# Optimization experiments

Hardware: AMD Instinct MI355X
Metric: run time of the kernel (lower is better)

The kernel has to match this reference:

```python
import jax, jax.numpy as jnp
import numpy as np
from jax import lax

E = 10        # embed_dim
SEQ = 4000    # input_frame (sample_length=40)
G = 800       # group
F = 5         # frames_in_group
B = 16
VOCAB = 8192


def _conv2d(x, w, b):
    # x: [B, C, H, W], w: [O, I, 3, 3], padding=1 -> SAME
    y = lax.conv_general_dilated(x, w, (1, 1), 'SAME',
                                 dimension_numbers=('NCHW', 'OIHW', 'NCHW'))
    return y + b[None, :, None, None]


def _conv1d_k1(x, w, b):
    # Conv1d(seq, seq, kernel=1): x [B, S, L], w [S_out, S_in]
    return jnp.einsum('oi,bil->bol', w, x) + b[None, :, None]


def _linear(x, w, b):
    # torch Linear: w [out, in]
    return x @ w.T + b


def setup_inputs() -> dict:
    key = jax.random.key(0)
    ks = jax.random.split(key, 24)
    s = 0.02
    inp = {
        'X': jax.random.randint(ks[0], (B, SEQ, 15), 0, VOCAB),
        'emb_table': jax.random.normal(ks[1], (VOCAB, E), jnp.float32),
        'w_dwc_lsp': jax.random.normal(ks[2], (G, G, 3, 3), jnp.float32) * s,
        'b_dwc_lsp': jnp.zeros((G,), jnp.float32),
        'w_dwc_other': jax.random.normal(ks[3], (G, G, 3, 3), jnp.float32) * s,
        'b_dwc_other': jnp.zeros((G,), jnp.float32),
        'w_local': jax.random.normal(ks[4], (SEQ, SEQ), jnp.float32) * s,
        'b_local': jnp.zeros((SEQ,), jnp.float32),
        'w_global': jax.random.normal(ks[5], (SEQ, SEQ), jnp.float32) * s,
        'b_global': jnp.zeros((SEQ,), jnp.float32),
        'w_gq': jax.random.normal(ks[6], (4 * E, 4 * E), jnp.float32) * s,
        'b_gq': jnp.zeros((4 * E,), jnp.float32),
        'w_cq': jax.random.normal(ks[7], (4 * E, 4 * E), jnp.float32) * s,
        'b_cq': jnp.zeros((4 * E,), jnp.float32),
        'w_pq': jax.random.normal(ks[8], (4 * E, 3 * E), jnp.float32) * s,
        'b_pq': jnp.zeros((4 * E,), jnp.float32),
        'w_lk': jax.random.normal(ks[9], (4 * E, 4 * E), jnp.float32) * s,
        'b_lk': jnp.zeros((4 * E,), jnp.float32),
        'w_lv': jax.random.normal(ks[10], (4 * E, 4 * E), jnp.float32) * s,
        'b_lv': jnp.zeros((4 * E,), jnp.float32),
        'w_cls': jax.random.normal(ks[11], (1, SEQ * 4 * E * 3), jnp.float32) * 0.001,
        'b_cls': jnp.zeros((1,), jnp.float32),
        'bn_w': jnp.ones((1,), jnp.float32),
        'bn_b': jnp.zeros((1,), jnp.float32),
    }
    return inp


def reference(X, emb_table, w_dwc_lsp, b_dwc_lsp, w_dwc_other, b_dwc_other,
              w_local, b_local, w_global, b_global,
              w_gq, b_gq, w_cq, b_cq, w_pq, b_pq,
              w_lk, b_lk, w_lv, b_lv, w_cls, b_cls, bn_w, bn_b):
    batch, seq, cw = X.shape
    gamma = jnp.float32(0.8)
    pk = jnp.array([0, 0, 0, 0, 1, 3, 1, 2, 3, 2, 3, 1, 2, 3, 3], jnp.float32)
    D = jnp.repeat(gamma ** pk, E)  # [150]

    Xe = emb_table[X].reshape(batch, seq, cw * E) * D  # [B, S, 150]
    ch = Xe.reshape(batch, seq, cw, E)                  # 15 chunks of E

    lsp = ch[:, :, jnp.array([0, 1, 2, 3])].reshape(batch, seq, 4 * E)
    pitch = ch[:, :, jnp.array([4, 5, 10])].reshape(batch, seq, 3 * E)
    code = ch[:, :, jnp.array([6, 7, 11, 12])].reshape(batch, seq, 4 * E)
    gain = ch[:, :, jnp.array([8, 13, 9, 14])].reshape(batch, seq, 4 * E)

    conv_lsp = _conv2d(lsp.reshape(batch, G, F, 4 * E), w_dwc_lsp, b_dwc_lsp).reshape(batch, seq, 4 * E)
    conv_pitch = _conv2d(pitch.reshape(batch, G, F, 3 * E), w_dwc_other, b_dwc_other).reshape(batch, seq, 3 * E)
    conv_code = _conv2d(code.reshape(batch, G, F, 4 * E), w_dwc_other, b_dwc_other).reshape(batch, seq, 4 * E)
    conv_gain = _conv2d(gain.reshape(batch, G, F, 4 * E), w_dwc_other, b_dwc_other).reshape(batch, seq, 4 * E)

    conv_lsp = _conv1d_k1(conv_lsp, w_local, b_local)
    conv_pitch = _conv1d_k1(conv_pitch, w_local, b_local)
    conv_code = _conv1d_k1(conv_code, w_local, b_local)
    conv_gain = _conv1d_k1(conv_gain, w_local, b_local)

    gain_q = _linear(conv_gain, w_gq, b_gq)    # [B, S, 40]
    pitch_q = _linear(conv_pitch, w_pq, b_pq)  # [B, S, 40]
    code_q = _linear(conv_code, w_cq, b_cq)    # [B, S, 40]
    lsp_k = _linear(conv_lsp, w_lk, b_lk)
    lsp_v = _linear(conv_lsp, w_lv, b_lv)

    # Q @ K^T @ V with no softmax: associate as Q @ (K^T V), O(S*d^2)
    kv = jnp.einsum('bsd,bse->bde', lsp_k, lsp_v)  # [B, 40, 40]
    out_gain = jnp.einsum('bsd,bde->bse', gain_q, kv) + lsp
    out_pitch = jnp.einsum('bsd,bde->bse', pitch_q, kv) + lsp
    out_code = jnp.einsum('bsd,bde->bse', code_q, kv) + lsp

    atten_out = jnp.concatenate([out_gain, out_pitch, out_code], -1)  # [B, S, 120]
    gf = _conv1d_k1(atten_out, w_global, b_global).reshape(batch, -1)  # [B, 480000]

    y = gf @ w_cls.T + b_cls  # [B, 1]
    # BatchNorm1d(1) in eval mode: running_mean=0, running_var=1
    eps = jnp.float32(1e-5)
    y = y * (bn_w / jnp.sqrt(1.0 + eps)) + bn_b
    return jax.nn.sigmoid(y)
```

## Files before the change

kernel.cpp:

```cpp
#include <hip/hip_runtime.h>
#include <hip/hip_bf16.h>

typedef _Float16 f16;
typedef __attribute__((ext_vector_type(8))) _Float16 half8;
typedef __attribute__((ext_vector_type(4))) _Float16 half4;
typedef __attribute__((ext_vector_type(4))) float f32x4;

static const int BN = 16, SEQN = 4000;

__device__ __forceinline__ void gload_lds(f16* lds, const f16* g) {
  __builtin_amdgcn_global_load_lds((const __attribute__((address_space(1))) unsigned int*)g,
                                   (__attribute__((address_space(3))) unsigned int*)lds, 16, 0, 0);
}

__device__ __forceinline__ int xcd_swz(int orig, int nwg) {
  int q = nwg >> 3, r = nwg & 7, x = orig & 7, o = orig >> 3;
  return (x < r ? x * (q + 1) : r * (q + 1) + (x - r) * q) + o;
}

__device__ __forceinline__ void body_wconv(char* SM, int o,
    const float* __restrict__ w_dwc_l, f16* __restrict__ wp_lsp) {
  float* sh = (float*)SM;
  int t = threadIdx.x;
  for (int p4 = t; p4 < 1800; p4 += 256)
    *(f32x4*)&sh[p4 * 4] = *(const f32x4*)&w_dwc_l[(long)o * 7200 + p4 * 4];
  __syncthreads();
  for (int p = t; p < 7296; p += 256) {
    int seg = p / 2432, r = p - seg * 2432;
    f16 v = (f16)0.f;
    if (r < 2400) { int de = r / 800, gi = r - de * 800; v = (f16)sh[gi * 9 + seg * 3 + de]; }
    wp_lsp[(long)o * 7296 + p] = v;
  }
}

__device__ __forceinline__ void body_wlocal(char* SM, int s,
    const float* __restrict__ w_local, f16* __restrict__ wlp) {
  float* sh = (float*)SM;
  int t = threadIdx.x;
  for (int p = t; p < 4000; p += 256) {
    int g = p / 5, f = p - g * 5;
    sh[f * 808 + g] = w_local[(long)s * 4000 + p];
  }
  __syncthreads();
  for (int p = t; p < 4096; p += 256) {
    f16 v = (f16)0.f;
    if (p < 4000) { int f = p / 800, g = p - f * 800; v = (f16)sh[f * 808 + g]; }
    wlp[(long)s * 4096 + p] = v;
  }
}

__device__ __forceinline__ void body_wcT(char* SM, int id,
    const float* __restrict__ w_cls, f16* __restrict__ wcT) {
  float (*tile)[33] = (float(*)[33])SM;
  int t = threadIdx.x;
  int c0 = (id % 4) * 32, r0 = (id / 4) * 32;
  int tx = t & 31, ty = t >> 5;
  for (int i = ty; i < 32; i += 8) {
    int r = r0 + i, c = c0 + tx;
    tile[i][tx] = (r < 4000 && c < 120) ? w_cls[(long)r * 120 + c] : 0.f;
  }
  __syncthreads();
  for (int i = ty; i < 32; i += 8) {
    int c = c0 + i, r = r0 + tx;
    if (c < 128 && r < 4000) wcT[(long)c * 4000 + r] = (f16)(tile[tx][i] * 1024.f);
  }
}

__device__ __forceinline__ void body_woT(char* SM, int id,
    const float* __restrict__ in, f16* __restrict__ out) {
  float (*sh)[293] = (float(*)[293])SM;
  int bg = id % 25, bgi = id / 25;
  int g0 = bg * 32, gi0 = bgi * 32;
  int t = threadIdx.x;
  for (int p = t; p < 2304; p += 256) {
    int gl = p / 72, q4 = p % 72;
    *(f32x4*)&sh[gl][q4 * 4] = *(const f32x4*)&in[(long)(g0 + gl) * 7200 + gi0 * 9 + q4 * 4];
  }
  __syncthreads();
  for (int p = t; p < 9216; p += 256) {
    int gl = p & 31, q = p >> 5;
    int gil = q & 31, z = q >> 5;
    out[(long)z * 640000 + (gi0 + gil) * 800 + g0 + gl] = (f16)sh[gl][gil * 9 + z];
  }
}

__device__ __forceinline__ void body_gather(char* SM, int bid,
    const int* __restrict__ X, const float* __restrict__ emb,
    f16* __restrict__ P_lsp, f16* __restrict__ P_pit,
    f16* __restrict__ P_cod, f16* __restrict__ P_gai,
    float* __restrict__ lsp32) {
  int* sx_ = (int*)SM;
  float* slsp = (float*)(SM + 9600);
  const float scale[15] = {1.f,1.f,1.f,1.f,0.8f,0.512f,0.8f,0.64f,0.512f,0.64f,0.512f,0.8f,0.64f,0.512f,0.512f};
  const int br[15] = {0,0,0,0,1,1,2,2,3,3,1,2,2,3,3};
  const int po[15] = {0,1,2,3,0,1,0,1,0,2,2,2,3,1,3};
  int t = threadIdx.x;
  int b = bid / 25, gc = bid % 25;
  int g0 = gc * 32, s0 = g0 * 5;
  const int* xbase = X + ((long)b * SEQN + s0) * 15;
  for (int p = t; p < 600; p += 256)
    *(f32x4*)&sx_[p * 4] = *(const f32x4*)&xbase[p * 4];
  __syncthreads();
  for (int it = t; it < 2400; it += 256) {
    int gl = it & 31, q = it >> 5, f = q % 5, c = q / 5;
    int idx = sx_[(gl * 5 + f) * 15 + c];
    const float* er = emb + (long)idx * 10;
    int ty = br[c], p = po[c];
    f16* P = (ty == 0) ? P_lsp : (ty == 1) ? P_pit : (ty == 2) ? P_cod : P_gai;
    int Wp = (ty == 1) ? 32 : 42;
    f16* base = P + ((long)((f + 1) * 16 + b) * Wp + (1 + p * 10)) * 800 + g0 + gl;
    float sc = scale[c];
#pragma unroll
    for (int j = 0; j < 10; j++) {
      float v = er[j] * sc;
      base[(long)j * 800] = (f16)v;
      if (ty == 0) slsp[(gl * 5 + f) * 41 + p * 10 + j] = v;
    }
  }
  __syncthreads();
  float* ldst = lsp32 + ((long)b * SEQN + s0) * 40;
  for (int p = t; p < 6400; p += 256) {
    int row = p / 40, col = p - row * 40;
    ldst[p] = slsp[row * 41 + col];
  }
}

__device__ __forceinline__ void body_c1(char* SM, int blk,
    const float* __restrict__ wcls, const float* __restrict__ bg,
    float* __restrict__ c1p) {
  float* red = (float*)SM;
  int t = threadIdx.x;
  float s = 0.f;
  for (long i = (long)blk * 256 + t; i < 480000; i += (long)120 * 256)
    s += wcls[i] * bg[i / 120];
  red[t] = s; __syncthreads();
  for (int o = 128; o > 0; o >>= 1) { if (t < o) red[t] += red[t + o]; __syncthreads(); }
  if (t == 0) c1p[blk] = red[0];
}

__device__ __forceinline__ void body_conv(char* SM, int id,
    const f16* __restrict__ P, const f16* __restrict__ wp, f16* __restrict__ Cp) {
  f16* Asb = (f16*)SM;
  f16* Bsb = Asb + 8192;
  int lin = xcd_swz(id % 175, 175);
  int z = id / 175;
  int df = z >> 1, hf = z & 1;
  int nx = lin % 7, my = lin / 7;
  int m0 = my * 128, n0 = nx * 128;
  Cp += (long)z * 2560000;
  int t = threadIdx.x;
  int gslot = (t & 3) ^ ((t >> 3) & 3);
  const f16 *ap[2], *bp[2];
#pragma unroll
  for (int q = 0; q < 2; q++) {
    int row = q * 64 + (t >> 2);
    int m = m0 + row;
    int f = m / 640, rem = m % 640, b = rem / 40, e = rem % 40;
    ap[q] = P + ((long)((f + df) * 16 + b) * 42 + e) * 800 + hf * 1216 + gslot * 8;
    bp[q] = wp + (long)(n0 + row) * 7296 + df * 2432 + hf * 1216 + gslot * 8;
  }
  int lane = t & 63, wv = t >> 6, l15 = lane & 15, kg = lane >> 4;
  int wm = (wv >> 1) * 64, wn = (wv & 1) * 64;
  int so = (kg ^ ((l15 >> 1) & 3)) << 3;
  f32x4 acc[4][4] = {};
  gload_lds(&Asb[t * 8], ap[0]); gload_lds(&Asb[2048 + t * 8], ap[1]);
  gload_lds(&Bsb[t * 8], bp[0]); gload_lds(&Bsb[2048 + t * 8], bp[1]);
  __syncthreads();
  int cur = 0;
  for (int kt = 0; kt < 38; kt++) {
    if (kt + 1 < 38) {
      int o = (kt + 1) * 32, nb = cur ^ 1;
      gload_lds(&Asb[nb * 4096 + t * 8], ap[0] + o); gload_lds(&Asb[nb * 4096 + 2048 + t * 8], ap[1] + o);
      gload_lds(&Bsb[nb * 4096 + t * 8], bp[0] + o); gload_lds(&Bsb[nb * 4096 + 2048 + t * 8], bp[1] + o);
    }
    half8 av[4], bv[4];
#pragma unroll
    for (int i = 0; i < 4; i++) av[i] = *(const half8*)&Asb[cur * 4096 + (wm + i * 16 + l15) * 32 + so];
#pragma unroll
    for (int j = 0; j < 4; j++) bv[j] = *(const half8*)&Bsb[cur * 4096 + (wn + j * 16 + l15) * 32 + so];
#pragma unroll
    for (int i = 0; i < 4; i++)
#pragma unroll
      for (int j = 0; j < 4; j++)
        acc[i][j] = __builtin_amdgcn_mfma_f32_16x16x32_f16(av[i], bv[j], acc[i][j], 0, 0, 0);
    __syncthreads();
    cur ^= 1;
  }
#pragma unroll
  for (int i = 0; i < 4; i++) {
    int mb = m0 + wm + i * 16 + kg * 4;
#pragma unroll
    for (int j = 0; j < 4; j++) {
      int n = n0 + wn + j * 16 + l15;
      if (n >= 800) continue;
      f32x4 d = acc[i][j];
#pragma unroll
      for (int r = 0; r < 4; r++)
        Cp[(long)(mb + r) * 800 + n] = (f16)d[r];
    }
  }
}

template <int OUTF16>
__device__ __forceinline__ void body_gemm128(char* SM, int x, int ky, int z,
    const f16* __restrict__ A, int lda, const f16* __restrict__ Bm, int ldb,
    float* __restrict__ C, f16* __restrict__ C16, int ldc,
    int gx, int nwg, int nkt, int KTtot, long cslice, long az, long bz, long cz,
    int Mreal, int Nreal, int Aclamp) {
  f16* Asb = (f16*)SM;
  f16* Bsb = Asb + 8192;
  A += (long)z * az;
  Bm += (long)z * bz;
  if (OUTF16) C16 += (long)z * cz + (long)ky * cslice;
  else C += (long)z * cz + (long)ky * cslice;
  int lin = xcd_swz(x, nwg);
  int nx = lin % gx, my = lin / gx;
  int m0 = my * 128, n0 = nx * 128;
  int kt0 = ky * nkt;
  int ktn = nkt; if (kt0 + ktn > KTtot) ktn = KTtot - kt0;
  int t = threadIdx.x;
  int gslot = (t & 3) ^ ((t >> 3) & 3);
  const f16 *ap[2], *bp[2];
#pragma unroll
  for (int q = 0; q < 2; q++) {
    int row = q * 64 + (t >> 2);
    int ra = m0 + row; if (ra >= Aclamp) ra = Aclamp - 1;
    ap[q] = A + (long)ra * lda + (long)kt0 * 32 + gslot * 8;
    bp[q] = Bm + (long)(n0 + row) * ldb + (long)kt0 * 32 + gslot * 8;
  }
  int lane = t & 63, wv = t >> 6, l15 = lane & 15, kg = lane >> 4;
  int wm = (wv >> 1) * 64, wn = (wv & 1) * 64;
  int so = (kg ^ ((l15 >> 1) & 3)) << 3;
  f32x4 acc[4][4] = {};
  gload_lds(&Asb[t * 8], ap[0]); gload_lds(&Asb[2048 + t * 8], ap[1]);
  gload_lds(&Bsb[t * 8], bp[0]); gload_lds(&Bsb[2048 + t * 8], bp[1]);
  __syncthreads();
  int cur = 0;
  for (int kt = 0; kt < ktn; kt++) {
    if (kt + 1 < ktn) {
      int o = (kt + 1) * 32, nb = cur ^ 1;
      gload_lds(&Asb[nb * 4096 + t * 8], ap[0] + o); gload_lds(&Asb[nb * 4096 + 2048 + t * 8], ap[1] + o);
      gload_lds(&Bsb[nb * 4096 + t * 8], bp[0] + o); gload_lds(&Bsb[nb * 4096 + 2048 + t * 8], bp[1] + o);
    }
    half8 av[4], bv[4];
#pragma unroll
    for (int i = 0; i < 4; i++) av[i] = *(const half8*)&Asb[cur * 4096 + (wm + i * 16 + l15) * 32 + so];
#pragma unroll
    for (int j = 0; j < 4; j++) bv[j] = *(const half8*)&Bsb[cur * 4096 + (wn + j * 16 + l15) * 32 + so];
#pragma unroll
    for (int i = 0; i < 4; i++)
#pragma unroll
      for (int j = 0; j < 4; j++)
        acc[i][j] = __builtin_amdgcn_mfma_f32_16x16x32_f16(av[i], bv[j], acc[i][j], 0, 0, 0);
    __syncthreads();
    cur ^= 1;
  }
#pragma unroll
  for (int i = 0; i < 4; i++) {
    int mb = m0 + wm + i * 16 + kg * 4;
#pragma unroll
    for (int j = 0; j < 4; j++) {
      int n = n0 + wn + j * 16 + l15;
      if (n >= Nreal) continue;
      f32x4 d = acc[i][j];
#pragma unroll
      for (int r = 0; r < 4; r++) {
        int m = mb + r;
        if (m >= Mreal) continue;
        if (OUTF16) C16[(long)m * ldc + n] = (f16)d[r];
        else C[(long)m * ldc + n] = d[r];
      }
    }
  }
}

__device__ __forceinline__ void body_tn(char* SM, int id,
    const f16* __restrict__ A, int lda, const float* __restrict__ B,
    const f16* __restrict__ B16, int ldb,
    float* __restrict__ C, int ldc, int nkt, int KTtot, long cslice,
    int Mreal, int Nreal) {
  f16* As = (f16*)SM;
  f16* Bs = As + 4096;
  int n0 = (id & 31) * 128;
  int ky = id >> 5;
  int kt0 = ky * nkt;
  int ktn = nkt; if (kt0 + ktn > KTtot) ktn = KTtot - kt0;
  C += (long)ky * cslice;
  int t = threadIdx.x;
  int gslot = (t & 3) ^ ((t >> 3) & 3);
  const f16 *ap0, *ap1;
  {
    int r0 = t >> 2, r1 = 64 + (t >> 2);
    if (r0 >= Mreal) r0 = Mreal - 1;
    if (r1 >= Mreal) r1 = Mreal - 1;
    ap0 = A + (long)r0 * lda + (long)kt0 * 32 + gslot * 8;
    ap1 = A + (long)r1 * lda + (long)kt0 * 32 + gslot * 8;
  }
  int lane = t & 63, wv = t >> 6;
  int wm = (wv >> 1) * 64, wn = (wv & 1) * 64;
  int l15 = lane & 15, kg = lane >> 4;
  int so = (kg ^ ((l15 >> 1) & 3)) << 3;
  f32x4 acc[4][4] = {};
  for (int kt = 0; kt < ktn; kt++) {
    f16 rb[4][4];
    int nli[4], kqi[4];
#pragma unroll
    for (int i = 0; i < 4; i++) {
      int idd = i * 256 + t;
      nli[i] = idd & 127; kqi[i] = idd >> 7;
      int gn = n0 + nli[i]; if (gn >= Nreal) gn = Nreal - 1;
      long kb = ((long)(kt0 + kt) * 32 + kqi[i] * 4);
#pragma unroll
      for (int j = 0; j < 4; j++)
        rb[i][j] = B16 ? B16[(kb + j) * ldb + gn] : (f16)B[(kb + j) * ldb + gn];
    }
    __syncthreads();
    gload_lds(&As[t * 8], ap0 + kt * 32);
    gload_lds(&As[2048 + t * 8], ap1 + kt * 32);
#pragma unroll
    for (int i = 0; i < 4; i++) {
      half4 h = {rb[i][0], rb[i][1], rb[i][2], rb[i][3]};
      *(half4*)&Bs[nli[i] * 36 + kqi[i] * 4] = h;
    }
    __syncthreads();
    half8 av[4], bv[4];
#pragma unroll
    for (int i = 0; i < 4; i++) {
      av[i] = *(const half8*)(&As[(wm + i * 16 + l15) * 32 + so]);
      bv[i] = *(const half8*)(&Bs[(wn + i * 16 + l15) * 36 + kg * 8]);
    }
#pragma unroll
    for (int i = 0; i < 4; i++)
#pragma unroll
      for (int j = 0; j < 4; j++)
        acc[i][j] = __builtin_amdgcn_mfma_f32_16x16x32_f16(av[i], bv[j], acc[i][j], 0, 0, 0);
  }
#pragma unroll
  for (int i = 0; i < 4; i++) {
    int mb = wm + i * 16 + kg * 4;
#pragma unroll
    for (int j = 0; j < 4; j++) {
      int n = n0 + wn + j * 16 + l15;
      if (n >= Nreal) continue;
      f32x4 d = acc[i][j];
#pragma unroll
      for (int r = 0; r < 4; r++) {
        int m = mb + r;
        if (m >= Mreal) continue;
        C[(long)m * ldc + n] = d[r];
      }
    }
  }
}

__device__ __forceinline__ void body_co_red(long gid,
    const f16* __restrict__ Cp, const float* __restrict__ bias, f16* __restrict__ co) {
  if (gid >= 640000) return;
  int m = gid / 200, n4 = (gid % 200) * 4;
  long o = (long)m * 800 + n4;
  f32x4 s = *(const f32x4*)&bias[n4];
#pragma unroll
  for (int z = 0; z < 6; z++) {
    half4 h = *(const half4*)&Cp[(long)z * 2560000 + o];
    s += (f32x4){(float)h[0], (float)h[1], (float)h[2], (float)h[3]};
  }
  int f = m / 640, r2 = m % 640;
  half4 hh = {(f16)s[0], (f16)s[1], (f16)s[2], (f16)s[3]};
  *(half4*)&co[(long)r2 * 4000 + f * 800 + n4] = hh;
}

__device__ __forceinline__ void body_vred(int idb, int MODE,
    const float* __restrict__ vp, float* __restrict__ vout, f16* __restrict__ tout) {
  int x = idb & 15, ec = idb >> 4;
  int s = x * 256 + threadIdx.x;
  if (s >= 4000) return;
  int g = s / 5, f = s % 5;
  int scol = (MODE == 0) ? s : (f * 800 + g);
  float sums[40];
#pragma unroll
  for (int eo = 0; eo < 40; eo++) {
    int e = ec * 40 + eo;
    float sum = 0.f;
#pragma unroll
    for (int z = 0; z < 10; z++) sum += vp[(long)z * 480000 + (long)e * 4000 + scol];
    sums[eo] = sum;
    if (MODE == 0) tout[(long)e * 4000 + s] = (f16)sum;
    else tout[(long)(f * 120 + e) * 832 + g] = (f16)sum;
  }
#pragma unroll
  for (int q = 0; q < 10; q++)
    *(f32x4*)&vout[(long)s * 120 + ec * 40 + q * 4] = *(f32x4*)&sums[q * 4];
}

__device__ __forceinline__ void body_cl_red(long gid,
    const f16* __restrict__ Clp, const float* __restrict__ bl, float* __restrict__ cl) {
  if (gid >= 640000) return;
  int m = gid / 160, n4 = (gid % 160) * 4;
  long o = (long)m * 640 + n4;
  float b = bl[m];
  f32x4 s = {b, b, b, b};
#pragma unroll
  for (int z = 0; z < 4; z++) {
    half4 h = *(const half4*)&Clp[(long)z * 2560000 + o];
    s += (f32x4){(float)h[0], (float)h[1], (float)h[2], (float)h[3]};
  }
  *(f32x4*)&cl[o] = s;
}

__device__ __forceinline__ void body_resid(char* SM, int chunk, int b,
    const float* __restrict__ lsp32, const float* __restrict__ vmat,
    float* __restrict__ rpart) {
  float* red = (float*)SM;
  int t = threadIdx.x;
  int s0 = chunk * 160;
  float y = 0.f;
  for (int idx = t; idx < 1600; idx += 256) {
    int sr = idx / 10, d4 = idx % 10;
    const float* lp = lsp32 + ((long)b * SEQN + s0 + sr) * 40 + d4 * 4;
    const float* vp = vmat + (long)(s0 + sr) * 120 + d4 * 4;
    f32x4 l = *(const f32x4*)lp;
    f32x4 vs = *(const f32x4*)vp + *(const f32x4*)(vp + 40) + *(const f32x4*)(vp + 80);
    y += l[0] * vs[0] + l[1] * vs[1] + l[2] * vs[2] + l[3] * vs[3];
  }
  red[t] = y; __syncthreads();
  for (int o = 128; o > 0; o >>= 1) { if (t < o) red[t] += red[t + o]; __syncthreads(); }
  if (t == 0) rpart[b * 25 + chunk] = red[0];
}

__device__ __forceinline__ void body_kv(char* SM, int chunk, int b,
    const float* __restrict__ cl, const float* __restrict__ wlk, const float* __restrict__ blk,
    const float* __restrict__ wlv, const float* __restrict__ blv, float* __restrict__ kvp) {
  float* s_wk = (float*)SM;
  float* s_wv = s_wk + 1600;
  float* s_cl = s_wv + 1600;
  float* s_k  = s_cl + 320;
  float* s_v  = s_k + 320;
  int t = threadIdx.x;
  for (int p = t; p < 1600; p += 256) { s_wk[p] = wlk[p]; s_wv[p] = wlv[p]; }
  float acc[7] = {0.f, 0.f, 0.f, 0.f, 0.f, 0.f, 0.f};
  for (int c8 = 0; c8 < 20; c8++) {
    int sb = chunk * 160 + c8 * 8;
    __syncthreads();
    for (int p = t; p < 320; p += 256) {
      int sl = p / 40, e = p % 40;
      s_cl[sl * 40 + e] = cl[(long)(sb + sl) * 640 + b * 40 + e];
    }
    __syncthreads();
    for (int p = t; p < 640; p += 256) {
      int half = p / 320, q = p % 320, sl = q / 40, d = q % 40;
      const float* w = half ? s_wv : s_wk;
      float r = half ? blv[d] : blk[d];
      for (int e = 0; e < 40; e++) r += w[d * 40 + e] * s_cl[sl * 40 + e];
      if (half) s_v[sl * 40 + d] = r; else s_k[sl * 40 + d] = r;
    }
    __syncthreads();
    int ai = 0;
    for (int p = t; p < 1600; p += 256, ai++) {
      int d = p / 40, e = p % 40;
      float a = acc[ai];
      for (int sl = 0; sl < 8; sl++) a += s_k[sl * 40 + d] * s_v[sl * 40 + e];
      acc[ai] = a;
    }
  }
  int ai = 0;
  for (int p = t; p < 1600; p += 256, ai++)
    kvp[((long)(b * 25 + chunk)) * 1600 + p] = acc[ai];
}

__device__ __forceinline__ void body_consts(char* SM, int e,
    const float* __restrict__ Vt, const float* __restrict__ vmat,
    const float* __restrict__ bconv, const float* __restrict__ blocal,
    float* __restrict__ cbblv, float* __restrict__ svv) {
  float* r1 = (float*)SM;
  float* r2 = r1 + 256;
  int t = threadIdx.x;
  float a = 0.f, b = 0.f;
  for (int s = t; s < 4000; s += 256) {
    a += bconv[s / 5] * Vt[(long)s * 120 + e] + blocal[s] * vmat[(long)s * 120 + e];
    b += vmat[(long)s * 120 + e];
  }
  r1[t] = a; r2[t] = b; __syncthreads();
  for (int o = 128; o > 0; o >>= 1) {
    if (t < o) { r1[t] += r1[t + o]; r2[t] += r2[t + o]; }
    __syncthreads();
  }
  if (t == 0) { cbblv[e] = r1[0]; svv[e] = r2[0]; }
}

__device__ __forceinline__ void body_fold(long c8,
    const float* __restrict__ A9, f16* __restrict__ Bp) {
  long p = c8 * 8;
  if (p >= 7 * 120 * 2496) return;
  int fp = p / 299520;
  int r = p % 299520;
  int eg = r / 2496, k2 = r % 2496;
  int zk = k2 / 832, kk = k2 % 832;
  half8 h = {};
  if (kk < 800) {
#pragma unroll
    for (int j = 0; j < 8; j++) {
      float s = 0.f;
#pragma unroll
      for (int dh = 0; dh < 3; dh++) {
        int f = fp - dh;
        if (f >= 0 && f < 5)
          s += A9[((long)(dh * 3 + zk) * 640 + f * 120 + eg) * 800 + kk + j];
      }
      h[j] = (f16)s;
    }
  }
  *(half8*)&Bp[p] = h;
}

__device__ __forceinline__ void body_kvred(long gid,
    const float* __restrict__ kvp, float* __restrict__ kv) {
  if (gid >= 16 * 1600) return;
  int b = gid / 1600, p = gid % 1600;
  float s = 0.f;
  for (int c = 0; c < 25; c++) s += kvp[((long)(b * 25 + c)) * 1600 + p];
  kv[gid] = s;
}

__device__ __forceinline__ void body_U(char* SM, int id,
    const f16* __restrict__ Pg, const f16* __restrict__ Pp, const f16* __restrict__ Pc,
    const f16* __restrict__ Bp, float* __restrict__ Upart) {
  f16* Asb = (f16*)SM;
  f16* Bsb = Asb + 8192;
  int m0 = (id % 28) * 64;
  int y = id / 28, fp = y / 3, zk = y % 3;
  const f16* P; int seg0, jw, Wp, e0;
  if (m0 < 640)       { seg0 = 0;    jw = 40; Wp = 42; e0 = 0;  P = Pg; }
  else if (m0 < 1152) { seg0 = 640;  jw = 30; Wp = 32; e0 = 40; P = Pp; }
  else                { seg0 = 1152; jw = 40; Wp = 42; e0 = 80; P = Pc; }
  P += (long)fp * 16 * Wp * 800;
  int t = threadIdx.x;
  int gslot = (t & 7) ^ ((t >> 3) & 7);
  const f16 *ap[2], *bp[2];
#pragma unroll
  for (int q = 0; q < 2; q++) {
    int row = q * 32 + (t >> 3);
    int l = m0 + row - seg0; if (l >= 16 * jw) l = 0;
    ap[q] = P + ((long)(l / jw) * Wp + (l % jw)) * 800 + (long)zk * 800 + gslot * 8;
    int brow = row; if (e0 + brow > 119) brow = 119 - e0;
    bp[q] = Bp + ((long)fp * 120 + e0 + brow) * 2496 + zk * 832 + gslot * 8;
  }
  int lane = t & 63, wv = t >> 6, l15 = lane & 15, kg = lane >> 4;
  int sx = l15 & 7;
  f32x4 acc[3] = {};
  gload_lds(&Asb[t * 8], ap[0]); gload_lds(&Asb[2048 + t * 8], ap[1]);
  gload_lds(&Bsb[t * 8], bp[0]); gload_lds(&Bsb[2048 + t * 8], bp[1]);
  __syncthreads();
  int cur = 0;
  for (int kt = 0; kt < 13; kt++) {
    if (kt + 1 < 13) {
      int o = (kt + 1) * 64, nb = cur ^ 1;
      gload_lds(&Asb[nb * 4096 + t * 8], ap[0] + o); gload_lds(&Asb[nb * 4096 + 2048 + t * 8], ap[1] + o);
      gload_lds(&Bsb[nb * 4096 + t * 8], bp[0] + o); gload_lds(&Bsb[nb * 4096 + 2048 + t * 8], bp[1] + o);
    }
#pragma unroll
    for (int ks = 0; ks < 2; ks++) {
      int so = ((ks * 4 + kg) ^ sx) << 3;
      half8 av = *(const half8*)&Asb[cur * 4096 + (wv * 16 + l15) * 64 + so];
#pragma unroll
      for (int j = 0; j < 3; j++) {
        half8 bv = *(const half8*)&Bsb[cur * 4096 + (j * 16 + l15) * 64 + so];
        acc[j] = __builtin_amdgcn_mfma_f32_16x16x32_f16(av, bv, acc[j], 0, 0, 0);
      }
    }
    __syncthreads();
    cur ^= 1;
  }
#pragma unroll
  for (int j = 0; j < 3; j++) {
    int n = j * 16 + l15;
    if (n >= 40) continue;
    f32x4 d = acc[j];
#pragma unroll
    for (int r = 0; r < 4; r++) {
      int m = m0 + wv * 16 + kg * 4 + r;
      if (m - seg0 >= 16 * jw) continue;
      Upart[((long)y * 1792 + m) * 40 + n] = d[r];
    }
  }
}

__device__ __forceinline__ void body_ured(long gid,
    const float* __restrict__ Upart, const float* __restrict__ cbblv,
    float* __restrict__ Ufin) {
  if (gid >= 1792 * 40) return;
  int m = gid / 40, e = gid % 40;
  int e0 = m < 640 ? 0 : (m < 1152 ? 40 : 80);
  float s = cbblv[e0 + e];
  for (int y = 0; y < 21; y++) s += Upart[(long)y * 71680 + gid];
  Ufin[gid] = s;
}

__global__ __launch_bounds__(256) void k_phase0(
    const float* w_local, f16* wlp, const float* w_dwc_l, f16* wp_lsp,
    const float* w_cls, f16* wcT,
    const int* X, const float* emb, f16* P_lsp, f16* P_pit, f16* P_cod, f16* P_gai,
    float* lsp32, const float* b_global, float* c1p,
    const float* w_dwc_o, f16* woT) {
  __shared__ __align__(16) char SM[37504];
  int bid = blockIdx.x;
  if (bid < 4000) body_wlocal(SM, bid, w_local, wlp);
  else if (bid < 4800) body_wconv(SM, bid - 4000, w_dwc_l, wp_lsp);
  else if (bid < 5300) body_wcT(SM, bid - 4800, w_cls, wcT);
  else if (bid < 5700) body_gather(SM, bid - 5300, X, emb, P_lsp, P_pit, P_cod, P_gai, lsp32);
  else if (bid < 5820) body_c1(SM, bid - 5700, w_cls, b_global, c1p);
  else body_woT(SM, bid - 5820, w_dwc_o, woT);
}

__global__ __launch_bounds__(256) void k_phase1(
    const f16* P_lsp, const f16* wp_lsp, f16* Cp,
    const f16* wcT, const float* w_global, float* vpart) {
  __shared__ __align__(16) char SM[32768];
  int bid = blockIdx.x;
  if (bid < 1050) body_conv(SM, bid, P_lsp, wp_lsp, Cp);
  else body_tn(SM, bid - 1050, wcT, 4000, w_global, nullptr, 4000, vpart, 4000, 13, 125, 480000L, 120, 4000);
}

__global__ __launch_bounds__(256) void k_phase2(
    const f16* Cp, const float* b_dwc_l, f16* co,
    const float* vpart, float* vmat, f16* vT) {
  int bid = blockIdx.x;
  if (bid < 2500) body_co_red((long)bid * 256 + threadIdx.x, Cp, b_dwc_l, co);
  else body_vred(bid - 2500, 0, vpart, vmat, vT);
}

__global__ __launch_bounds__(256) void k_phase3(
    const f16* wlp, const f16* co, f16* Clp,
    const f16* vT, float* vpart,
    const float* lsp32, const float* vmat, float* rpart) {
  __shared__ __align__(16) char SM[32768];
  int bid = blockIdx.x;
  if (bid < 640) body_gemm128<1>(SM, bid % 160, bid / 160, 0, wlp, 4096, co, 4000, nullptr, Clp, 640,
                                 5, 160, 32, 128, 2560000L, 0, 0, 0, 4000, 640, 4000);
  else if (bid < 960) body_tn(SM, bid - 640, vT, 4000, nullptr, wlp, 4096, vpart, 4000, 13, 125, 480000L, 120, 4000);
  else { int id = bid - 960; body_resid(SM, id % 25, id / 25, lsp32, vmat, rpart); }
}

__global__ __launch_bounds__(256) void k_phase4(
    const f16* Clp, const float* b_local, float* cl,
    const float* vpart, float* Vt, f16* vtT) {
  int bid = blockIdx.x;
  if (bid < 2500) body_cl_red((long)bid * 256 + threadIdx.x, Clp, b_local, cl);
  else body_vred(bid - 2500, 1, vpart, Vt, vtT);
}

__global__ __launch_bounds__(256) void k_phase5(
    const float* cl, const float* w_lk, const float* b_lk,
    const float* w_lv, const float* b_lv, float* kvp,
    const f16* vtT, const f16* woT, float* A9,
    const float* Vt, const float* vmat, const float* b_dwc_o, const float* b_local,
    float* cbblv, float* svv) {
  __shared__ __align__(16) char SM[32768];
  int bid = blockIdx.x;
  if (bid < 400) body_kv(SM, bid % 25, bid / 25, cl, w_lk, b_lk, w_lv, b_lv, kvp);
  else if (bid < 715) { int id = bid - 400; body_gemm128<0>(SM, id % 35, 0, id / 35, vtT, 832, woT, 800, A9, nullptr, 800,
                                                             7, 35, 26, 26, 0L, 0, 640000, 512000, 600, 800, 600); }
  else body_consts(SM, bid - 715, Vt, vmat, b_dwc_o, b_local, cbblv, svv);
}

__global__ __launch_bounds__(256) void k_phase6(
    const float* A9, f16* Bp, const float* kvp, float* kvb) {
  int bid = blockIdx.x;
  if (bid < 1024) body_fold((long)bid * 256 + threadIdx.x, A9, Bp);
  else body_kvred((long)(bid - 1024) * 256 + threadIdx.x, kvp, kvb);
}

__global__ __launch_bounds__(256) void k_phase7(
    const f16* P_gai, const f16* P_pit, const f16* P_cod,
    const f16* Bp, float* Upart) {
  __shared__ __align__(16) char SM[32768];
  body_U(SM, blockIdx.x, P_gai, P_pit, P_cod, Bp, Upart);
}

__global__ __launch_bounds__(256) void k_phase8(
    const float* Upart, const float* cbblv, float* Ufin) {
  body_ured((long)blockIdx.x * 256 + threadIdx.x, Upart, cbblv, Ufin);
}

__global__ __launch_bounds__(256) void k_final(
    const float* __restrict__ Ufin, const float* __restrict__ kvb,
    const float* __restrict__ rpart,
    const float* __restrict__ wgq, const float* __restrict__ wpq, const float* __restrict__ wcq,
    const float* __restrict__ bgq, const float* __restrict__ bpq, const float* __restrict__ bcq,
    const float* __restrict__ svv, const float* __restrict__ c1p,
    const float* __restrict__ bcls, const float* __restrict__ bnw,
    const float* __restrict__ bnb, float* __restrict__ out) {
  __shared__ float s_kv[1600], s_U[4800], s_w[4400], s_bq[120], s_sv[120], s_red[256];
  int b = blockIdx.x, t = threadIdx.x;
  for (int p = t; p < 1600; p += 256) {
    s_kv[p] = kvb[b * 1600 + p];
    s_w[p] = wgq[p];
    s_w[2800 + p] = wcq[p];
  }
  for (int p = t; p < 1200; p += 256) s_w[1600 + p] = wpq[p];
  for (int p = t; p < 4800; p += 256) {
    int tt = p / 1600, r = p % 1600, j = r / 40, e = r % 40;
    float uv = 0.f;
    if (tt == 0) uv = Ufin[(b * 40 + j) * 40 + e];
    else if (tt == 1) { if (j < 30) uv = Ufin[(640 + b * 30 + j) * 40 + e]; }
    else uv = Ufin[(1152 + b * 40 + j) * 40 + e];
    s_U[p] = uv;
  }
  if (t < 40) { s_bq[t] = bgq[t]; s_bq[40 + t] = bpq[t]; s_bq[80 + t] = bcq[t]; }
  for (int p = t; p < 120; p += 256) s_sv[p] = svv[p];
  __syncthreads();
  float y = 0.f;
  for (int p = t; p < 4800; p += 256) {
    int tt = p / 1600, q = p % 1600, d = q / 40, e = q % 40;
    float T = 0.f;
    if (tt == 0) {
      for (int j = 0; j < 40; j++) T += s_w[d * 40 + j] * s_U[j * 40 + e];
    } else if (tt == 1) {
      for (int j = 0; j < 30; j++) T += s_w[1600 + d * 30 + j] * s_U[1600 + j * 40 + e];
    } else {
      for (int j = 0; j < 40; j++) T += s_w[2800 + d * 40 + j] * s_U[3200 + j * 40 + e];
    }
    y += s_kv[d * 40 + e] * (T + s_bq[tt * 40 + d] * s_sv[tt * 40 + e]);
  }
  for (int p = t; p < 25; p += 256) y += rpart[b * 25 + p];
  s_red[t] = y; __syncthreads();
  for (int o = 128; o > 0; o >>= 1) { if (t < o) s_red[t] += s_red[t + o]; __syncthreads(); }
  if (t == 0) {
    float c1 = bcls[0];
    for (int i = 0; i < 120; i++) c1 += c1p[i];
    float yy = s_red[0] * (1.f / 1024.f) + c1;
    yy = yy * (bnw[0] * rsqrtf(1.f + 1e-5f)) + bnb[0];
    out[b] = 1.f / (1.f + expf(-yy));
  }
}

extern "C" void kernel_launch(void* const* d_in, const int* in_sizes, int n_in,
                              void* d_out, int out_size, void* d_ws, size_t ws_size,
                              hipStream_t stream) {
  const int*   X        = (const int*)d_in[0];
  const float* emb      = (const float*)d_in[1];
  const float* w_dwc_l  = (const float*)d_in[2];
  const float* b_dwc_l  = (const float*)d_in[3];
  const float* w_dwc_o  = (const float*)d_in[4];
  const float* b_dwc_o  = (const float*)d_in[5];
  const float* w_local  = (const float*)d_in[6];
  const float* b_local  = (const float*)d_in[7];
  const float* w_global = (const float*)d_in[8];
  const float* b_global = (const float*)d_in[9];
  const float* w_gq = (const float*)d_in[10];
  const float* b_gq = (const float*)d_in[11];
  const float* w_cq = (const float*)d_in[12];
  const float* b_cq = (const float*)d_in[13];
  const float* w_pq = (const float*)d_in[14];
  const float* b_pq = (const float*)d_in[15];
  const float* w_lk = (const float*)d_in[16];
  const float* b_lk = (const float*)d_in[17];
  const float* w_lv = (const float*)d_in[18];
  const float* b_lv = (const float*)d_in[19];
  const float* w_cls = (const float*)d_in[20];
  const float* b_cls = (const float*)d_in[21];
  const float* bn_w = (const float*)d_in[22];
  const float* bn_b = (const float*)d_in[23];
  float* out = (float*)d_out;

  char* ws = (char*)d_ws;
  size_t off = 0;
  auto alloc = [&](size_t bytes) -> void* {
    off = (off + 255) & ~(size_t)255;
    void* p = ws + off; off += bytes; return p;
  };

  const size_t sz_p40 = (size_t)7 * 16 * 42 * 800 * 2;
  const size_t sz_p30 = (size_t)7 * 16 * 32 * 800 * 2;
  f16* P_lsp = (f16*)alloc(sz_p40 + 256);
  f16* P_pit = (f16*)alloc(sz_p30 + 256);
  f16* P_cod = (f16*)alloc(sz_p40 + 256);
  f16* P_gai = (f16*)alloc(sz_p40 + 256);
  float* lsp32 = (float*)alloc((size_t)16 * 4000 * 40 * 4);
  f16* wp_lsp = (f16*)alloc((size_t)896 * 7296 * 2);
  f16* wlp    = (f16*)alloc((size_t)4000 * 4096 * 2 + 256);
  f16* wcT    = (f16*)alloc((size_t)128 * 4000 * 2);
  f16* vT     = (f16*)alloc((size_t)128 * 4000 * 2);
  f16* co     = (f16*)alloc((size_t)640 * 4000 * 2 + 256);
  float* cl   = (float*)alloc((size_t)4000 * 640 * 4);
  float* vmat  = (float*)alloc((size_t)480000 * 4);
  float* Vt    = (float*)alloc((size_t)480000 * 4);
  f16* vtT   = (f16*)alloc((size_t)640 * 832 * 2 + 256);
  f16* Bp    = (f16*)alloc((size_t)7 * 120 * 2496 * 2);
  float* Upart = (float*)alloc((size_t)21 * 1792 * 40 * 4);
  float* Ufin  = (float*)alloc((size_t)1792 * 40 * 4);
  float* cbblv = (float*)alloc(120 * 4);
  float* svv   = (float*)alloc(120 * 4);
  float* kvp  = (float*)alloc((size_t)400 * 1600 * 4);
  float* kvb  = (float*)alloc((size_t)16 * 1600 * 4);
  float* c1p  = (float*)alloc(120 * 4);
  float* rpart = (float*)alloc(400 * 4);
  f16* woT = (f16*)alloc(((size_t)9 * 640000 + 76800) * 2);
  float* vpart = (float*)alloc((size_t)10 * 480000 * 4);
  char* arena = (char*)alloc((size_t)32 * 1024 * 1024);
  f16* Cp   = (f16*)arena;
  f16* Clp  = (f16*)arena;
  float* A9 = (float*)arena;
  (void)ws_size; (void)in_sizes; (void)n_in; (void)out_size;

  hipMemsetAsync(P_lsp, 0, sz_p40, stream);
  hipMemsetAsync(P_pit, 0, sz_p30, stream);
  hipMemsetAsync(P_cod, 0, sz_p40, stream);
  hipMemsetAsync(P_gai, 0, sz_p40, stream);
  hipMemsetAsync(vtT, 0, (size_t)640 * 832 * 2, stream);

  k_phase0<<<6445, 256, 0, stream>>>(w_local, wlp, w_dwc_l, wp_lsp, w_cls, wcT,
                                     X, emb, P_lsp, P_pit, P_cod, P_gai,
                                     lsp32, b_global, c1p, w_dwc_o, woT);
  k_phase1<<<1370, 256, 0, stream>>>(P_lsp, wp_lsp, Cp, wcT, w_global, vpart);
  k_phase2<<<2548, 256, 0, stream>>>(Cp, b_dwc_l, co, vpart, vmat, vT);
  k_phase3<<<1360, 256, 0, stream>>>(wlp, co, Clp, vT, vpart, lsp32, vmat, rpart);
  k_phase4<<<2548, 256, 0, stream>>>(Clp, b_local, cl, vpart, Vt, vtT);
  k_phase5<<<835, 256, 0, stream>>>(cl, w_lk, b_lk, w_lv, b_lv, kvp,
                                    vtT, woT, A9, Vt, vmat, b_dwc_o, b_local, cbblv, svv);
  k_phase6<<<1124, 256, 0, stream>>>(A9, Bp, kvp, kvb);
  k_phase7<<<588, 256, 0, stream>>>(P_gai, P_pit, P_cod, Bp, Upart);
  k_phase8<<<280, 256, 0, stream>>>(Upart, cbblv, Ufin);
  k_final<<<16, 256, 0, stream>>>(Ufin, kvb, rpart,
                                  w_gq, w_pq, w_cq, b_gq, b_pq, b_cq,
                                  svv, c1p, b_cls, bn_w, bn_b, out);
}
```

Baseline: 470.8 us.

## Rebalance weight-prep work across phases to overlap with compute kernels

```diff
diff --git a/kernel.cpp b/kernel.cpp
--- a/kernel.cpp
+++ b/kernel.cpp
@@ -596,36 +596,37 @@
 }
 
 __global__ __launch_bounds__(256) void k_phase0(
-    const float* w_local, f16* wlp, const float* w_dwc_l, f16* wp_lsp,
-    const float* w_cls, f16* wcT,
+    const float* w_dwc_l, f16* wp_lsp, const float* w_cls, f16* wcT,
     const int* X, const float* emb, f16* P_lsp, f16* P_pit, f16* P_cod, f16* P_gai,
-    float* lsp32, const float* b_global, float* c1p,
+    float* lsp32, const float* b_global, float* c1p) {
+  __shared__ __align__(16) char SM[35840];
+  int bid = blockIdx.x;
+  if (bid < 800) body_wconv(SM, bid, w_dwc_l, wp_lsp);
+  else if (bid < 1300) body_wcT(SM, bid - 800, w_cls, wcT);
+  else if (bid < 1700) body_gather(SM, bid - 1300, X, emb, P_lsp, P_pit, P_cod, P_gai, lsp32);
+  else body_c1(SM, bid - 1700, w_cls, b_global, c1p);
+}
+
+__global__ __launch_bounds__(256) void k_phase1(
+    const f16* P_lsp, const f16* wp_lsp, f16* Cp,
+    const f16* wcT, const float* w_global, float* vpart,
+    const float* w_local, f16* wlp) {
+  __shared__ __align__(16) char SM[32768];
+  int bid = blockIdx.x;
+  if (bid < 1050) body_conv(SM, bid, P_lsp, wp_lsp, Cp);
+  else if (bid < 1370) body_tn(SM, bid - 1050, wcT, 4000, w_global, nullptr, 4000, vpart, 4000, 13, 125, 480000L, 120, 4000);
+  else body_wlocal(SM, bid - 1370, w_local, wlp);
+}
+
+__global__ __launch_bounds__(256) void k_phase2(
+    const f16* Cp, const float* b_dwc_l, f16* co,
+    const float* vpart, float* vmat, f16* vT,
     const float* w_dwc_o, f16* woT) {
   __shared__ __align__(16) char SM[37504];
   int bid = blockIdx.x;
-  if (bid < 4000) body_wlocal(SM, bid, w_local, wlp);
-  else if (bid < 4800) body_wconv(SM, bid - 4000, w_dwc_l, wp_lsp);
-  else if (bid < 5300) body_wcT(SM, bid - 4800, w_cls, wcT);
-  else if (bid < 5700) body_gather(SM, bid - 5300, X, emb, P_lsp, P_pit, P_cod, P_gai, lsp32);
-  else if (bid < 5820) body_c1(SM, bid - 5700, w_cls, b_global, c1p);
-  else body_woT(SM, bid - 5820, w_dwc_o, woT);
-}
-
-__global__ __launch_bounds__(256) void k_phase1(
-    const f16* P_lsp, const f16* wp_lsp, f16* Cp,
-    const f16* wcT, const float* w_global, float* vpart) {
-  __shared__ __align__(16) char SM[32768];
-  int bid = blockIdx.x;
-  if (bid < 1050) body_conv(SM, bid, P_lsp, wp_lsp, Cp);
-  else body_tn(SM, bid - 1050, wcT, 4000, w_global, nullptr, 4000, vpart, 4000, 13, 125, 480000L, 120, 4000);
-}
-
-__global__ __launch_bounds__(256) void k_phase2(
-    const f16* Cp, const float* b_dwc_l, f16* co,
-    const float* vpart, float* vmat, f16* vT) {
-  int bid = blockIdx.x;
   if (bid < 2500) body_co_red((long)bid * 256 + threadIdx.x, Cp, b_dwc_l, co);
-  else body_vred(bid - 2500, 0, vpart, vmat, vT);
+  else if (bid < 2548) body_vred(bid - 2500, 0, vpart, vmat, vT);
+  else body_woT(SM, bid - 2548, w_dwc_o, woT);
 }
 
 __global__ __launch_bounds__(256) void k_phase3(
@@ -808,11 +809,12 @@
   hipMemsetAsync(P_gai, 0, sz_p40, stream);
   hipMemsetAsync(vtT, 0, (size_t)640 * 832 * 2, stream);
 
-  k_phase0<<<6445, 256, 0, stream>>>(w_local, wlp, w_dwc_l, wp_lsp, w_cls, wcT,
+  k_phase0<<<1820, 256, 0, stream>>>(w_dwc_l, wp_lsp, w_cls, wcT,
                                      X, emb, P_lsp, P_pit, P_cod, P_gai,
-                                     lsp32, b_global, c1p, w_dwc_o, woT);
-  k_phase1<<<1370, 256, 0, stream>>>(P_lsp, wp_lsp, Cp, wcT, w_global, vpart);
-  k_phase2<<<2548, 256, 0, stream>>>(Cp, b_dwc_l, co, vpart, vmat, vT);
+                                     lsp32, b_global, c1p);
+  k_phase1<<<5370, 256, 0, stream>>>(P_lsp, wp_lsp, Cp, wcT, w_global, vpart,
+                                     w_local, wlp);
+  k_phase2<<<3173, 256, 0, stream>>>(Cp, b_dwc_l, co, vpart, vmat, vT, w_dwc_o, woT);
   k_phase3<<<1360, 256, 0, stream>>>(wlp, co, Clp, vT, vpart, lsp32, vmat, rpart);
   k_phase4<<<2548, 256, 0, stream>>>(Clp, b_local, cl, vpart, Vt, vtT);
   k_phase5<<<835, 256, 0, stream>>>(cl, w_lk, b_lk, w_lv, b_lv, kvp,
```

After: 501.0 us. 6.4% more time.
